# Kernel tuning notes

Hardware: AMD Instinct MI355X
Metric: run time of the kernel (lower is better)

The kernel has to match this reference:

```python
import jax, jax.numpy as jnp
import numpy as np

B, T, H, E, D, K = 4, 4096, 2048, 8, 1024, 2

def setup_inputs() -> dict:
    key = jax.random.key(0)
    ks = jax.random.split(key, 7)
    x  = jax.random.normal(ks[0], (B, T, H), dtype=jnp.float32)
    Wr = jax.random.normal(ks[1], (H, E), dtype=jnp.float32) * (1.0 / np.sqrt(H))
    br = jnp.zeros((E,), dtype=jnp.float32)
    We = jax.random.normal(ks[2], (E, H, D), dtype=jnp.float32) * (1.0 / np.sqrt(H))
    be = jnp.zeros((E, D), dtype=jnp.float32)
    Wc = jax.random.normal(ks[3], (D, H), dtype=jnp.float32) * (1.0 / np.sqrt(D))
    bc = jnp.zeros((H,), dtype=jnp.float32)
    return {"x": x, "Wr": Wr, "br": br, "We": We, "be": be, "Wc": Wc, "bc": bc}

def reference(x, Wr, br, We, be, Wc, bc):
    # Router: [B,T,H] @ [H,E] -> [B,T,E]
    router_logits = jnp.einsum('bth,he->bte', x, Wr) + br
    scores = jax.nn.softmax(router_logits, axis=-1)
    # top-k over experts (sorted descending, like torch.topk)
    topk_scores, topk_idx = jax.lax.top_k(scores, K)  # [B,T,K]
    # Dense all-expert linear: [B,T,E,D]
    expert_outs = jnp.einsum('bth,ehd->bted', x, We) + be
    # Gather the chosen experts per token: [B,T,K,D]
    gather_idx = jnp.broadcast_to(topk_idx[..., None], (B, T, K, D))
    chosen = jnp.take_along_axis(expert_outs, gather_idx, axis=2)
    # Weighted sum over top-k: [B,T,D]
    weighted = jnp.sum(chosen * topk_scores[..., None], axis=2)
    # Combine: [B,T,D] @ [D,H] -> [B,T,H]
    return jnp.einsum('btd,dh->bth', weighted, Wc) + bc
```

## Files before the change

### kernel.cpp

```cpp
#include <hip/hip_runtime.h>
#include <hip/hip_bf16.h>

typedef float f32x4 __attribute__((ext_vector_type(4)));
typedef short bf16x8 __attribute__((ext_vector_type(8)));

#define M_NT 16
#define M_OFF 17
#define M_TBL 32
#define MAX_TILES 264
#define NCHUNK 1024

__device__ __forceinline__ void gload16(const void* g, void* l) {
  __builtin_amdgcn_global_load_lds(
      (const __attribute__((address_space(1))) void*)g,
      (__attribute__((address_space(3))) void*)l, 16, 0, 0);
}

__device__ __forceinline__ float bf2f(unsigned short u) {
  union { unsigned int i; float f; } v; v.i = ((unsigned int)u) << 16; return v.f;
}
__device__ __forceinline__ unsigned short f2bf(float f) {
  __hip_bfloat16 h = __float2bfloat16(f);
  return __builtin_bit_cast(unsigned short, h);
}

__global__ void transpose_cvt(const float* __restrict__ src,
                              unsigned short* __restrict__ dst, int R, int C) {
  __shared__ float tile[32][33];
  int b = blockIdx.z;
  int c0 = blockIdx.x * 32, r0 = blockIdx.y * 32;
  src += (size_t)b * R * C;
  dst += (size_t)b * R * C;
  int tx = threadIdx.x, ty = threadIdx.y;
#pragma unroll
  for (int i = 0; i < 32; i += 8)
    tile[ty + i][tx] = src[(size_t)(r0 + ty + i) * C + c0 + tx];
  __syncthreads();
#pragma unroll
  for (int i = 0; i < 32; i += 8)
    dst[(size_t)(c0 + ty + i) * R + r0 + tx] = f2bf(tile[tx][ty + i]);
}

__global__ __launch_bounds__(256) void router_kernel(
    const float* __restrict__ x, const float* __restrict__ Wr,
    const float* __restrict__ br, unsigned short* __restrict__ xbf,
    float* __restrict__ scores, int* __restrict__ idx,
    int* __restrict__ blk_hist) {
  __shared__ int cnt[8];
  int tid = threadIdx.x, lane = tid & 63, w = tid >> 6;
  if (tid < 8) cnt[tid] = 0;
  __syncthreads();
  int t0 = blockIdx.x * 16 + w * 4;
  const float* xr = x + (size_t)t0 * 2048;
  unsigned short* xo = xbf + (size_t)t0 * 2048;
  float acc[4][8] = {};
#pragma unroll
  for (int j = 0; j < 8; ++j) {
    int h0 = j * 256 + lane * 4;
    float4 xv[4];
#pragma unroll
    for (int t = 0; t < 4; ++t) xv[t] = *(const float4*)(xr + (size_t)t * 2048 + h0);
#pragma unroll
    for (int t = 0; t < 4; ++t) {
      ushort4 p;
      p.x = f2bf(xv[t].x); p.y = f2bf(xv[t].y);
      p.z = f2bf(xv[t].z); p.w = f2bf(xv[t].w);
      *(ushort4*)(xo + (size_t)t * 2048 + h0) = p;
    }
    const float4* wp = (const float4*)(Wr + (size_t)h0 * 8);
#pragma unroll
    for (int c = 0; c < 4; ++c) {
      float4 w0 = wp[2 * c], w1 = wp[2 * c + 1];
      float xc0 = (c == 0) ? xv[0].x : (c == 1) ? xv[0].y : (c == 2) ? xv[0].z : xv[0].w;
      float xc1 = (c == 0) ? xv[1].x : (c == 1) ? xv[1].y : (c == 2) ? xv[1].z : xv[1].w;
      float xc2 = (c == 0) ? xv[2].x : (c == 1) ? xv[2].y : (c == 2) ? xv[2].z : xv[2].w;
      float xc3 = (c == 0) ? xv[3].x : (c == 1) ? xv[3].y : (c == 2) ? xv[3].z : xv[3].w;
      acc[0][0] += xc0 * w0.x; acc[0][1] += xc0 * w0.y; acc[0][2] += xc0 * w0.z; acc[0][3] += xc0 * w0.w;
      acc[0][4] += xc0 * w1.x; acc[0][5] += xc0 * w1.y; acc[0][6] += xc0 * w1.z; acc[0][7] += xc0 * w1.w;
      acc[1][0] += xc1 * w0.x; acc[1][1] += xc1 * w0.y; acc[1][2] += xc1 * w0.z; acc[1][3] += xc1 * w0.w;
      acc[1][4] += xc1 * w1.x; acc[1][5] += xc1 * w1.y; acc[1][6] += xc1 * w1.z; acc[1][7] += xc1 * w1.w;
      acc[2][0] += xc2 * w0.x; acc[2][1] += xc2 * w0.y; acc[2][2] += xc2 * w0.z; acc[2][3] += xc2 * w0.w;
      acc[2][4] += xc2 * w1.x; acc[2][5] += xc2 * w1.y; acc[2][6] += xc2 * w1.z; acc[2][7] += xc2 * w1.w;
      acc[3][0] += xc3 * w0.x; acc[3][1] += xc3 * w0.y; acc[3][2] += xc3 * w0.z; acc[3][3] += xc3 * w0.w;
      acc[3][4] += xc3 * w1.x; acc[3][5] += xc3 * w1.y; acc[3][6] += xc3 * w1.z; acc[3][7] += xc3 * w1.w;
    }
  }
#pragma unroll
  for (int t = 0; t < 4; ++t)
#pragma unroll
    for (int e = 0; e < 8; ++e)
#pragma unroll
      for (int off = 32; off > 0; off >>= 1)
        acc[t][e] += __shfl_xor(acc[t][e], off);
  if (lane < 4) {
    int t = t0 + lane;
    float l[8];
#pragma unroll
    for (int e = 0; e < 8; ++e) {
      float v = (lane == 0) ? acc[0][e] : (lane == 1) ? acc[1][e]
              : (lane == 2) ? acc[2][e] : acc[3][e];
      l[e] = v + br[e];
    }
    float mx = l[0];
#pragma unroll
    for (int e = 1; e < 8; ++e) mx = fmaxf(mx, l[e]);
    float se = 0.f;
#pragma unroll
    for (int e = 0; e < 8; ++e) se += __expf(l[e] - mx);
    float inv = 1.f / se;
    int e1 = 0; float b1 = l[0];
#pragma unroll
    for (int e = 1; e < 8; ++e) if (l[e] > b1) { b1 = l[e]; e1 = e; }
    int e2 = -1; float b2 = -1e30f;
#pragma unroll
    for (int e = 0; e < 8; ++e) if (e != e1 && l[e] > b2) { b2 = l[e]; e2 = e; }
    idx[2 * t] = e1; idx[2 * t + 1] = e2;
    scores[2 * t] = __expf(b1 - mx) * inv;
    scores[2 * t + 1] = __expf(b2 - mx) * inv;
    atomicAdd(&cnt[e1], 1);
    atomicAdd(&cnt[e2], 1);
  }
  __syncthreads();
  if (tid < 8) blk_hist[blockIdx.x * 8 + tid] = cnt[tid];
}

__global__ __launch_bounds__(512) void scan_kernel(
    const int* __restrict__ blk_hist, int* __restrict__ chunk_base,
    int* __restrict__ meta, int* __restrict__ rowlist) {
  __shared__ int stot[8], soff[8];
  int tid = threadIdx.x, lane = tid & 63, e = tid >> 6;
  int running = 0;
  for (int g = 0; g < NCHUNK / 64; ++g) {
    int c = g * 64 + lane;
    int v = blk_hist[c * 8 + e];
    int orig = v;
#pragma unroll
    for (int off = 1; off < 64; off <<= 1) {
      int n = __shfl_up(v, off);
      if (lane >= off) v += n;
    }
    chunk_base[c * 8 + e] = running + v - orig;
    running += __shfl(v, 63);
  }
  if (lane == 0) stot[e] = running;
  __syncthreads();
  if (tid == 0) {
    int off = 0, nt = 0;
    int4* tbl = (int4*)(meta + M_TBL);
    for (int ee = 0; ee < 8; ++ee) {
      int c = stot[ee];
      meta[M_OFF + ee] = off; soff[ee] = off;
      int tiles = (c + 127) >> 7;
      for (int t = 0; t < tiles; ++t)
        tbl[nt++] = make_int4(ee, off + t * 128, min(128, c - t * 128), 0);
      off += tiles << 7;
    }
    meta[M_NT] = nt;
  }
  __syncthreads();
  for (int ee = 0; ee < 8; ++ee) {
    int c = stot[ee], end = ((c + 127) >> 7) << 7;
    for (int i = c + tid; i < end; i += 512) rowlist[soff[ee] + i] = 0;
  }
}

__global__ void scatter_kernel(const int* __restrict__ idx,
                               const int* __restrict__ chunk_base,
                               const int* __restrict__ meta,
                               int* __restrict__ rowlist) {
  int c = blockIdx.x, lane = threadIdx.x;
  int entry = c * 32 + lane;
  int e = (lane < 32) ? idx[entry] : -1;
#pragma unroll
  for (int ee = 0; ee < 8; ++ee) {
    unsigned long long m = __ballot(e == ee);
    if (e == ee) {
      int rank = __popcll(m & ((1ull << lane) - 1));
      rowlist[meta[M_OFF + ee] + chunk_base[c * 8 + ee] + rank] = entry;
    }
  }
}

__global__ __launch_bounds__(256) void expert_gemm(
    const unsigned short* __restrict__ xbf,
    const unsigned short* __restrict__ WeT,
    const float* __restrict__ be,
    const float* __restrict__ scores,
    const int* __restrict__ rowlist,
    const int* __restrict__ meta,
    unsigned short* __restrict__ z) {
  __shared__ short lA[128 * 32];
  __shared__ short lB[128 * 32];
  __shared__ int lrows[128];
  if ((int)blockIdx.y >= meta[M_NT]) return;
  int4 tt = ((const int4*)(meta + M_TBL))[blockIdx.y];
  int e = tt.x, base = tt.y, valid = tt.z;
  int n0 = blockIdx.x * 128;
  int tid = threadIdx.x, lane = tid & 63, w = tid >> 6;
  if (tid < 128) lrows[tid] = rowlist[base + tid];
  __syncthreads();
  int ch0 = 2 * w, ch1 = ch0 + 1;
  int sub = lane >> 2, colb = (lane & 3) * 8;
  int ra0 = lrows[ch0 * 16 + sub] >> 1;
  int ra1 = lrows[ch1 * 16 + sub] >> 1;
  const unsigned short* sA0 = xbf + (size_t)ra0 * 2048 + colb;
  const unsigned short* sA1 = xbf + (size_t)ra1 * 2048 + colb;
  const unsigned short* Bb = WeT + (size_t)e * 1024 * 2048;
  const unsigned short* sB0 = Bb + (size_t)(n0 + ch0 * 16 + sub) * 2048 + colb;
  const unsigned short* sB1 = Bb + (size_t)(n0 + ch1 * 16 + sub) * 2048 + colb;
  f32x4 acc[4][4] = {};
  int wr = (w >> 1) * 64, wc = (w & 1) * 64;
  int fl = lane & 15, q = lane >> 4;
  for (int k0 = 0; k0 < 2048; k0 += 32) {
    __syncthreads();
    gload16(sA0, lA + ch0 * 512);
    gload16(sA1, lA + ch1 * 512);
    gload16(sB0, lB + ch0 * 512);
    gload16(sB1, lB + ch1 * 512);
    sA0 += 32; sA1 += 32; sB0 += 32; sB1 += 32;
    __syncthreads();
    bf16x8 a[4], b[4];
#pragma unroll
    for (int i = 0; i < 4; ++i) a[i] = *(const bf16x8*)(lA + (wr + i * 16 + fl) * 32 + q * 8);
#pragma unroll
    for (int i = 0; i < 4; ++i) b[i] = *(const bf16x8*)(lB + (wc + i * 16 + fl) * 32 + q * 8);
#pragma unroll
    for (int mi = 0; mi < 4; ++mi)
#pragma unroll
      for (int ni = 0; ni < 4; ++ni)
        acc[mi][ni] = __builtin_amdgcn_mfma_f32_16x16x32_bf16(a[mi], b[ni], acc[mi][ni], 0, 0, 0);
  }
  float bev[4];
#pragma unroll
  for (int ni = 0; ni < 4; ++ni) bev[ni] = be[e * 1024 + n0 + wc + ni * 16 + fl];
#pragma unroll
  for (int mi = 0; mi < 4; ++mi)
#pragma unroll
    for (int r = 0; r < 4; ++r) {
      int row = wr + mi * 16 + q * 4 + r;
      if (row < valid) {
        int entry = lrows[row];
        float s = scores[entry];
        unsigned short* zr = z + (size_t)entry * 1024 + n0 + wc;
#pragma unroll
        for (int ni = 0; ni < 4; ++ni)
          zr[ni * 16 + fl] = f2bf((acc[mi][ni][r] + bev[ni]) * s);
      }
    }
}

__global__ void wsum_kernel(const unsigned short* __restrict__ z,
                            unsigned short* __restrict__ y) {
  size_t i = ((size_t)blockIdx.x * 256 + threadIdx.x) * 8;
  size_t t = i >> 10, d = i & 1023;
  int4 za = *(const int4*)(z + (t * 2) * 1024 + d);
  int4 zb = *(const int4*)(z + (t * 2 + 1) * 1024 + d);
  int4 r;
  const unsigned short* pa = (const unsigned short*)&za;
  const unsigned short* pb = (const unsigned short*)&zb;
  unsigned short* pr = (unsigned short*)&r;
#pragma unroll
  for (int j = 0; j < 8; ++j) pr[j] = f2bf(bf2f(pa[j]) + bf2f(pb[j]));
  *(int4*)(y + i) = r;
}

__global__ __launch_bounds__(256) void combine_gemm(
    const unsigned short* __restrict__ y,
    const unsigned short* __restrict__ WcT,
    const float* __restrict__ bc,
    float* __restrict__ out) {
  __shared__ short lA[128 * 32];
  __shared__ short lB[128 * 32];
  int tid = threadIdx.x, lane = tid & 63, w = tid >> 6;
  int m0 = blockIdx.y * 128, n0 = blockIdx.x * 128;
  int ch0 = 2 * w, ch1 = ch0 + 1;
  int sub = lane >> 2, colb = (lane & 3) * 8;
  const unsigned short* sA0 = y + (size_t)(m0 + ch0 * 16 + sub) * 1024 + colb;
  const unsigned short* sA1 = y + (size_t)(m0 + ch1 * 16 + sub) * 1024 + colb;
  const unsigned short* sB0 = WcT + (size_t)(n0 + ch0 * 16 + sub) * 1024 + colb;
  const unsigned short* sB1 = WcT + (size_t)(n0 + ch1 * 16 + sub) * 1024 + colb;
  f32x4 acc[4][4] = {};
  int wr = (w >> 1) * 64, wc = (w & 1) * 64;
  int fl = lane & 15, q = lane >> 4;
  for (int k0 = 0; k0 < 1024; k0 += 32) {
    __syncthreads();
    gload16(sA0, lA + ch0 * 512);
    gload16(sA1, lA + ch1 * 512);
    gload16(sB0, lB + ch0 * 512);
    gload16(sB1, lB + ch1 * 512);
    sA0 += 32; sA1 += 32; sB0 += 32; sB1 += 32;
    __syncthreads();
    bf16x8 a[4], b[4];
#pragma unroll
    for (int i = 0; i < 4; ++i) a[i] = *(const bf16x8*)(lA + (wr + i * 16 + fl) * 32 + q * 8);
#pragma unroll
    for (int i = 0; i < 4; ++i) b[i] = *(const bf16x8*)(lB + (wc + i * 16 + fl) * 32 + q * 8);
#pragma unroll
    for (int mi = 0; mi < 4; ++mi)
#pragma unroll
      for (int ni = 0; ni < 4; ++ni)
        acc[mi][ni] = __builtin_amdgcn_mfma_f32_16x16x32_bf16(a[mi], b[ni], acc[mi][ni], 0, 0, 0);
  }
  float bcv[4];
#pragma unroll
  for (int ni = 0; ni < 4; ++ni) bcv[ni] = bc[n0 + wc + ni * 16 + fl];
#pragma unroll
  for (int mi = 0; mi < 4; ++mi)
#pragma unroll
    for (int r = 0; r < 4; ++r) {
      int row = m0 + wr + mi * 16 + q * 4 + r;
      float* orow = out + (size_t)row * 2048 + n0 + wc;
#pragma unroll
      for (int ni = 0; ni < 4; ++ni) orow[ni * 16 + fl] = acc[mi][ni][r] + bcv[ni];
    }
}

extern "C" void kernel_launch(void* const* d_in, const int* in_sizes, int n_in,
                              void* d_out, int out_size, void* d_ws, size_t ws_size,
                              hipStream_t stream) {
  const float* x  = (const float*)d_in[0];
  const float* Wr = (const float*)d_in[1];
  const float* br = (const float*)d_in[2];
  const float* We = (const float*)d_in[3];
  const float* be = (const float*)d_in[4];
  const float* Wc = (const float*)d_in[5];
  const float* bc = (const float*)d_in[6];
  float* out = (float*)d_out;

  char* ws = (char*)d_ws;
  size_t o = 0;
  auto alloc = [&](size_t b) {
    char* p = ws + o;
    o = (o + b + 255) & ~(size_t)255;
    return p;
  };
  unsigned short* xbf = (unsigned short*)alloc(16384UL * 2048 * 2);
  unsigned short* WeT = (unsigned short*)alloc(8UL * 1024 * 2048 * 2);
  unsigned short* WcT = (unsigned short*)alloc(2048UL * 1024 * 2);
  unsigned short* z   = (unsigned short*)alloc(32768UL * 1024 * 2);
  unsigned short* yw  = (unsigned short*)alloc(16384UL * 1024 * 2);
  float* scores = (float*)alloc(32768UL * 4);
  int* idx      = (int*)alloc(32768UL * 4);
  int* rowlist  = (int*)alloc(33792UL * 4);
  int* meta     = (int*)alloc(8192);
  int* blk_hist = (int*)alloc(NCHUNK * 8 * 4);
  int* chunk_base = (int*)alloc(NCHUNK * 8 * 4);
  (void)ws_size; (void)in_sizes; (void)n_in; (void)out_size;

  hipLaunchKernelGGL(transpose_cvt, dim3(32, 64, 8), dim3(32, 8), 0, stream, We, WeT, 2048, 1024);
  hipLaunchKernelGGL(transpose_cvt, dim3(64, 32, 1), dim3(32, 8), 0, stream, Wc, WcT, 1024, 2048);
  hipLaunchKernelGGL(router_kernel, dim3(NCHUNK), dim3(256), 0, stream, x, Wr, br, xbf, scores, idx, blk_hist);
  hipLaunchKernelGGL(scan_kernel, dim3(1), dim3(512), 0, stream, blk_hist, chunk_base, meta, rowlist);
  hipLaunchKernelGGL(scatter_kernel, dim3(NCHUNK), dim3(64), 0, stream, idx, chunk_base, meta, rowlist);
  hipLaunchKernelGGL(expert_gemm, dim3(8, MAX_TILES), dim3(256), 0, stream,
                     xbf, WeT, be, scores, rowlist, meta, z);
  hipLaunchKernelGGL(wsum_kernel, dim3(8192), dim3(256), 0, stream, z, yw);
  hipLaunchKernelGGL(combine_gemm, dim3(16, 128), dim3(256), 0, stream, yw, WcT, bc, out);
}
```

Measured before the change: 433.0 us.

## Rewrite MoE GEMMs with 256x128 tiles, double-buffered swizzled LDS, and grouped block ordering

Both the expert and combine GEMMs now use 512-thread blocks computing 256x128 tiles with a K-step of 64. Global-to-LDS loads are double-buffered and overlapped with MFMA work through explicit vmcnt waits and raw barriers, and the LDS layout is XOR-swizzled to avoid bank conflicts. Block indices are remapped so consecutive blocks share tiles for better L2 reuse, and the router table moves to 256-row tiles, which changes padding and the rowlist size. This is meant to cut the per-k-step sync overhead and the global latency stalls of the old single-buffer 128x128 loop, at the cost of more registers and padding waste on small expert groups.

```diff
diff --git a/kernel.cpp b/kernel.cpp
--- a/kernel.cpp
+++ b/kernel.cpp
@@ -7,7 +7,7 @@
 #define M_NT 16
 #define M_OFF 17
 #define M_TBL 32
-#define MAX_TILES 264
+#define MAX_TILES 136
 #define NCHUNK 1024
 
 __device__ __forceinline__ void gload16(const void* g, void* l) {
@@ -23,6 +23,10 @@
   __hip_bfloat16 h = __float2bfloat16(f);
   return __builtin_bit_cast(unsigned short, h);
 }
+
+#define CBAR() do { asm volatile("" ::: "memory"); __builtin_amdgcn_s_barrier(); asm volatile("" ::: "memory"); } while (0)
+#define VMC3() asm volatile("s_waitcnt vmcnt(3)" ::: "memory")
+#define VMC0() asm volatile("s_waitcnt vmcnt(0)" ::: "memory")
 
 __global__ void transpose_cvt(const float* __restrict__ src,
                               unsigned short* __restrict__ dst, int R, int C) {
@@ -150,16 +154,16 @@
     for (int ee = 0; ee < 8; ++ee) {
       int c = stot[ee];
       meta[M_OFF + ee] = off; soff[ee] = off;
-      int tiles = (c + 127) >> 7;
+      int tiles = (c + 255) >> 8;
       for (int t = 0; t < tiles; ++t)
-        tbl[nt++] = make_int4(ee, off + t * 128, min(128, c - t * 128), 0);
-      off += tiles << 7;
+        tbl[nt++] = make_int4(ee, off + t * 256, min(256, c - t * 256), 0);
+      off += tiles << 8;
     }
     meta[M_NT] = nt;
   }
   __syncthreads();
   for (int ee = 0; ee < 8; ++ee) {
-    int c = stot[ee], end = ((c + 127) >> 7) << 7;
+    int c = stot[ee], end = ((c + 255) >> 8) << 8;
     for (int i = c + tid; i < end; i += 512) rowlist[soff[ee] + i] = 0;
   }
 }
@@ -181,7 +185,29 @@
   }
 }
 
-__global__ __launch_bounds__(256) void expert_gemm(
+
+#define RD_FRAGS(AB, BB) do { \
+  _Pragma("unroll") for (int m_ = 0; m_ < 8; ++m_) \
+    av[m_] = *(const bf16x8*)(aP + (AB) + m_ * 1024); \
+  _Pragma("unroll") for (int n_ = 0; n_ < 2; ++n_) \
+    bv[n_] = *(const bf16x8*)(bP + (BB) + n_ * 1024); \
+} while (0)
+
+#define MFMA16() do { \
+  __builtin_amdgcn_s_setprio(1); \
+  _Pragma("unroll") for (int m_ = 0; m_ < 8; ++m_) \
+  _Pragma("unroll") for (int n_ = 0; n_ < 2; ++n_) \
+    acc[m_][n_] = __builtin_amdgcn_mfma_f32_16x16x32_bf16(av[m_], bv[n_], acc[m_][n_], 0, 0, 0); \
+  __builtin_amdgcn_s_setprio(0); \
+} while (0)
+
+#define STAGE(BUFB, KOFF) do { \
+  gload16(pA0 + (KOFF), dA + (BUFB)); \
+  gload16(pA1 + (KOFF), dA + (BUFB) + 8192); \
+  gload16(pB0 + (KOFF), dBs + (BUFB)); \
+} while (0)
+
+__global__ __launch_bounds__(512, 4) void expert_gemm(
     const unsigned short* __restrict__ xbf,
     const unsigned short* __restrict__ WeT,
     const float* __restrict__ be,
@@ -189,64 +215,127 @@
     const int* __restrict__ rowlist,
     const int* __restrict__ meta,
     unsigned short* __restrict__ z) {
-  __shared__ short lA[128 * 32];
-  __shared__ short lB[128 * 32];
-  __shared__ int lrows[128];
-  if ((int)blockIdx.y >= meta[M_NT]) return;
-  int4 tt = ((const int4*)(meta + M_TBL))[blockIdx.y];
+  __shared__ char smem[49152];
+  __shared__ int lrows[256];
+  int nt = meta[M_NT];
+  int flat = blockIdx.y * 8 + blockIdx.x;
+  int work = (flat & 7) * 136 + (flat >> 3);
+  int tileid = work >> 3, nb = work & 7;
+  if (tileid >= nt) return;
+  int4 tt = ((const int4*)(meta + M_TBL))[tileid];
   int e = tt.x, base = tt.y, valid = tt.z;
-  int n0 = blockIdx.x * 128;
+  int n0 = nb * 128;
   int tid = threadIdx.x, lane = tid & 63, w = tid >> 6;
-  if (tid < 128) lrows[tid] = rowlist[base + tid];
-  __syncthreads();
-  int ch0 = 2 * w, ch1 = ch0 + 1;
-  int sub = lane >> 2, colb = (lane & 3) * 8;
-  int ra0 = lrows[ch0 * 16 + sub] >> 1;
-  int ra1 = lrows[ch1 * 16 + sub] >> 1;
-  const unsigned short* sA0 = xbf + (size_t)ra0 * 2048 + colb;
-  const unsigned short* sA1 = xbf + (size_t)ra1 * 2048 + colb;
-  const unsigned short* Bb = WeT + (size_t)e * 1024 * 2048;
-  const unsigned short* sB0 = Bb + (size_t)(n0 + ch0 * 16 + sub) * 2048 + colb;
-  const unsigned short* sB1 = Bb + (size_t)(n0 + ch1 * 16 + sub) * 2048 + colb;
-  f32x4 acc[4][4] = {};
-  int wr = (w >> 1) * 64, wc = (w & 1) * 64;
+  if (tid < 256) lrows[tid] = rowlist[base + tid];
+  __syncthreads();
+  int wm = w >> 2, wn = w & 3;
   int fl = lane & 15, q = lane >> 4;
-  for (int k0 = 0; k0 < 2048; k0 += 32) {
-    __syncthreads();
-    gload16(sA0, lA + ch0 * 512);
-    gload16(sA1, lA + ch1 * 512);
-    gload16(sB0, lB + ch0 * 512);
-    gload16(sB1, lB + ch1 * 512);
-    sA0 += 32; sA1 += 32; sB0 += 32; sB1 += 32;
-    __syncthreads();
-    bf16x8 a[4], b[4];
-#pragma unroll
-    for (int i = 0; i < 4; ++i) a[i] = *(const bf16x8*)(lA + (wr + i * 16 + fl) * 32 + q * 8);
-#pragma unroll
-    for (int i = 0; i < 4; ++i) b[i] = *(const bf16x8*)(lB + (wc + i * 16 + fl) * 32 + q * 8);
-#pragma unroll
-    for (int mi = 0; mi < 4; ++mi)
-#pragma unroll
-      for (int ni = 0; ni < 4; ++ni)
-        acc[mi][ni] = __builtin_amdgcn_mfma_f32_16x16x32_bf16(a[mi], b[ni], acc[mi][ni], 0, 0, 0);
-  }
-  float bev[4];
-#pragma unroll
-  for (int ni = 0; ni < 4; ++ni) bev[ni] = be[e * 1024 + n0 + wc + ni * 16 + fl];
-#pragma unroll
-  for (int mi = 0; mi < 4; ++mi)
+  int rA = tid >> 2;
+  int sl = ((tid & 3) ^ (rA & 3)) * 16;
+  const char* pA0 = (const char*)xbf + (size_t)(lrows[rA] >> 1) * 4096 + sl;
+  const char* pA1 = (const char*)xbf + (size_t)(lrows[rA + 128] >> 1) * 4096 + sl;
+  const char* pB0 = (const char*)WeT + ((size_t)e * 1024 + n0 + rA) * 4096 + sl;
+  char* dA  = smem + tid * 16;
+  char* dBs = smem + 16384 + tid * 16;
+  int swz = (fl & 3) << 4;
+  const char* aP = smem + (wm * 128 + fl) * 64 + ((q * 16) ^ swz);
+  const char* bP = smem + 16384 + (wn * 32 + fl) * 64 + ((q * 16) ^ swz);
+  STAGE(0, 0); STAGE(24576, 64);
+  VMC3(); CBAR();
+  f32x4 acc[8][2] = {};
+  bf16x8 av[8], bv[2];
+  const int NT = 64;
+  for (int t2 = 0; t2 < NT; t2 += 2) {
+    int koff = t2 * 64;
+    RD_FRAGS(0, 0);
+    MFMA16();
+    CBAR();
+    if (t2 + 2 < NT) { STAGE(0, koff + 128); VMC3(); } else { VMC0(); }
+    CBAR();
+    RD_FRAGS(24576, 24576);
+    MFMA16();
+    CBAR();
+    if (t2 + 3 < NT) { STAGE(24576, koff + 192); VMC3(); } else { VMC0(); }
+    CBAR();
+  }
+  float bev[2];
+#pragma unroll
+  for (int nc = 0; nc < 2; ++nc)
+    bev[nc] = be[e * 1024 + n0 + wn * 32 + nc * 16 + fl];
+#pragma unroll
+  for (int mi = 0; mi < 8; ++mi) {
+    int rowbase = wm * 128 + mi * 16 + q * 4;
 #pragma unroll
     for (int r = 0; r < 4; ++r) {
-      int row = wr + mi * 16 + q * 4 + r;
+      int row = rowbase + r;
       if (row < valid) {
         int entry = lrows[row];
         float s = scores[entry];
-        unsigned short* zr = z + (size_t)entry * 1024 + n0 + wc;
-#pragma unroll
-        for (int ni = 0; ni < 4; ++ni)
-          zr[ni * 16 + fl] = f2bf((acc[mi][ni][r] + bev[ni]) * s);
+        unsigned short* zr = z + (size_t)entry * 1024 + n0 + wn * 32 + fl;
+#pragma unroll
+        for (int nc = 0; nc < 2; ++nc)
+          zr[nc * 16] = f2bf((acc[mi][nc][r] + bev[nc]) * s);
       }
     }
+  }
+}
+
+__global__ __launch_bounds__(512, 4) void combine_gemm(
+    const unsigned short* __restrict__ y,
+    const unsigned short* __restrict__ WcT,
+    const float* __restrict__ bc,
+    float* __restrict__ out) {
+  __shared__ char smem[49152];
+  int flat = blockIdx.y * 8 + blockIdx.x;
+  int work = (flat & 7) * 128 + (flat >> 3);
+  int mtile = work >> 4, nb = work & 15;
+  int m0 = mtile * 256, n0 = nb * 128;
+  int tid = threadIdx.x, lane = tid & 63, w = tid >> 6;
+  int wm = w >> 2, wn = w & 3;
+  int fl = lane & 15, q = lane >> 4;
+  int rA = tid >> 2;
+  int sl = ((tid & 3) ^ (rA & 3)) * 16;
+  const char* pA0 = (const char*)y + (size_t)(m0 + rA) * 2048 + sl;
+  const char* pA1 = (const char*)y + (size_t)(m0 + rA + 128) * 2048 + sl;
+  const char* pB0 = (const char*)WcT + (size_t)(n0 + rA) * 2048 + sl;
+  char* dA  = smem + tid * 16;
+  char* dBs = smem + 16384 + tid * 16;
+  int swz = (fl & 3) << 4;
+  const char* aP = smem + (wm * 128 + fl) * 64 + ((q * 16) ^ swz);
+  const char* bP = smem + 16384 + (wn * 32 + fl) * 64 + ((q * 16) ^ swz);
+  STAGE(0, 0); STAGE(24576, 64);
+  VMC3(); CBAR();
+  f32x4 acc[8][2] = {};
+  bf16x8 av[8], bv[2];
+  const int NT = 32;
+  for (int t2 = 0; t2 < NT; t2 += 2) {
+    int koff = t2 * 64;
+    RD_FRAGS(0, 0);
+    MFMA16();
+    CBAR();
+    if (t2 + 2 < NT) { STAGE(0, koff + 128); VMC3(); } else { VMC0(); }
+    CBAR();
+    RD_FRAGS(24576, 24576);
+    MFMA16();
+    CBAR();
+    if (t2 + 3 < NT) { STAGE(24576, koff + 192); VMC3(); } else { VMC0(); }
+    CBAR();
+  }
+  float bcv[2];
+#pragma unroll
+  for (int nc = 0; nc < 2; ++nc)
+    bcv[nc] = bc[n0 + wn * 32 + nc * 16 + fl];
+#pragma unroll
+  for (int mi = 0; mi < 8; ++mi) {
+    int rowbase = m0 + wm * 128 + mi * 16 + q * 4;
+#pragma unroll
+    for (int r = 0; r < 4; ++r) {
+      float* orow = out + (size_t)(rowbase + r) * 2048 + n0 + wn * 32 + fl;
+#pragma unroll
+      for (int nc = 0; nc < 2; ++nc)
+        orow[nc * 16] = acc[mi][nc][r] + bcv[nc];
+    }
+  }
 }
 
 __global__ void wsum_kernel(const unsigned short* __restrict__ z,
@@ -262,57 +351,6 @@
 #pragma unroll
   for (int j = 0; j < 8; ++j) pr[j] = f2bf(bf2f(pa[j]) + bf2f(pb[j]));
   *(int4*)(y + i) = r;
-}
-
-__global__ __launch_bounds__(256) void combine_gemm(
-    const unsigned short* __restrict__ y,
-    const unsigned short* __restrict__ WcT,
-    const float* __restrict__ bc,
-    float* __restrict__ out) {
-  __shared__ short lA[128 * 32];
-  __shared__ short lB[128 * 32];
-  int tid = threadIdx.x, lane = tid & 63, w = tid >> 6;
-  int m0 = blockIdx.y * 128, n0 = blockIdx.x * 128;
-  int ch0 = 2 * w, ch1 = ch0 + 1;
-  int sub = lane >> 2, colb = (lane & 3) * 8;
-  const unsigned short* sA0 = y + (size_t)(m0 + ch0 * 16 + sub) * 1024 + colb;
-  const unsigned short* sA1 = y + (size_t)(m0 + ch1 * 16 + sub) * 1024 + colb;
-  const unsigned short* sB0 = WcT + (size_t)(n0 + ch0 * 16 + sub) * 1024 + colb;
-  const unsigned short* sB1 = WcT + (size_t)(n0 + ch1 * 16 + sub) * 1024 + colb;
-  f32x4 acc[4][4] = {};
-  int wr = (w >> 1) * 64, wc = (w & 1) * 64;
-  int fl = lane & 15, q = lane >> 4;
-  for (int k0 = 0; k0 < 1024; k0 += 32) {
-    __syncthreads();
-    gload16(sA0, lA + ch0 * 512);
-    gload16(sA1, lA + ch1 * 512);
-    gload16(sB0, lB + ch0 * 512);
-    gload16(sB1, lB + ch1 * 512);
-    sA0 += 32; sA1 += 32; sB0 += 32; sB1 += 32;
-    __syncthreads();
-    bf16x8 a[4], b[4];
-#pragma unroll
-    for (int i = 0; i < 4; ++i) a[i] = *(const bf16x8*)(lA + (wr + i * 16 + fl) * 32 + q * 8);
-#pragma unroll
-    for (int i = 0; i < 4; ++i) b[i] = *(const bf16x8*)(lB + (wc + i * 16 + fl) * 32 + q * 8);
-#pragma unroll
-    for (int mi = 0; mi < 4; ++mi)
-#pragma unroll
-      for (int ni = 0; ni < 4; ++ni)
-        acc[mi][ni] = __builtin_amdgcn_mfma_f32_16x16x32_bf16(a[mi], b[ni], acc[mi][ni], 0, 0, 0);
-  }
-  float bcv[4];
-#pragma unroll
-  for (int ni = 0; ni < 4; ++ni) bcv[ni] = bc[n0 + wc + ni * 16 + fl];
-#pragma unroll
-  for (int mi = 0; mi < 4; ++mi)
-#pragma unroll
-    for (int r = 0; r < 4; ++r) {
-      int row = m0 + wr + mi * 16 + q * 4 + r;
-      float* orow = out + (size_t)row * 2048 + n0 + wc;
-#pragma unroll
-      for (int ni = 0; ni < 4; ++ni) orow[ni * 16 + fl] = acc[mi][ni][r] + bcv[ni];
-    }
 }
 
 extern "C" void kernel_launch(void* const* d_in, const int* in_sizes, int n_in,
@@ -341,7 +379,7 @@
   unsigned short* yw  = (unsigned short*)alloc(16384UL * 1024 * 2);
   float* scores = (float*)alloc(32768UL * 4);
   int* idx      = (int*)alloc(32768UL * 4);
-  int* rowlist  = (int*)alloc(33792UL * 4);
+  int* rowlist  = (int*)alloc(36864UL * 4);
   int* meta     = (int*)alloc(8192);
   int* blk_hist = (int*)alloc(NCHUNK * 8 * 4);
   int* chunk_base = (int*)alloc(NCHUNK * 8 * 4);
@@ -352,8 +390,8 @@
   hipLaunchKernelGGL(router_kernel, dim3(NCHUNK), dim3(256), 0, stream, x, Wr, br, xbf, scores, idx, blk_hist);
   hipLaunchKernelGGL(scan_kernel, dim3(1), dim3(512), 0, stream, blk_hist, chunk_base, meta, rowlist);
   hipLaunchKernelGGL(scatter_kernel, dim3(NCHUNK), dim3(64), 0, stream, idx, chunk_base, meta, rowlist);
-  hipLaunchKernelGGL(expert_gemm, dim3(8, MAX_TILES), dim3(256), 0, stream,
+  hipLaunchKernelGGL(expert_gemm, dim3(8, MAX_TILES), dim3(512), 0, stream,
                      xbf, WeT, be, scores, rowlist, meta, z);
   hipLaunchKernelGGL(wsum_kernel, dim3(8192), dim3(256), 0, stream, z, yw);
-  hipLaunchKernelGGL(combine_gemm, dim3(16, 128), dim3(256), 0, stream, yw, WcT, bc, out);
-}
+  hipLaunchKernelGGL(combine_gemm, dim3(8, 128), dim3(512), 0, stream, yw, WcT, bc, out);
+}
```

Measured after the change: 395.1 us. 8.8% less time.

## Replace LDS-staged GEMMs with single-wave direct-register double-buffered MFMA kernels

Applied to the files above, without the earlier changes.

Both expert and combine GEMMs drop LDS staging and block-wide barriers. Each 64-thread wave now loads its own 128x64 operand fragments straight from global memory into registers, double-buffers them, and raises wave priority around the MFMA bursts. Expert tiles grow to 256 rows, and the flat grid is remapped so work spreads across XCDs. This removes synchronisation and LDS traffic, but gives up operand sharing between waves, so global/L2 load traffic and register pressure rise.

```diff
diff --git a/kernel.cpp b/kernel.cpp
--- a/kernel.cpp
+++ b/kernel.cpp
@@ -7,14 +7,8 @@
 #define M_NT 16
 #define M_OFF 17
 #define M_TBL 32
-#define MAX_TILES 264
+#define MAX_TILES 136
 #define NCHUNK 1024
-
-__device__ __forceinline__ void gload16(const void* g, void* l) {
-  __builtin_amdgcn_global_load_lds(
-      (const __attribute__((address_space(1))) void*)g,
-      (__attribute__((address_space(3))) void*)l, 16, 0, 0);
-}
 
 __device__ __forceinline__ float bf2f(unsigned short u) {
   union { unsigned int i; float f; } v; v.i = ((unsigned int)u) << 16; return v.f;
@@ -150,16 +144,16 @@
     for (int ee = 0; ee < 8; ++ee) {
       int c = stot[ee];
       meta[M_OFF + ee] = off; soff[ee] = off;
-      int tiles = (c + 127) >> 7;
+      int tiles = (c + 255) >> 8;
       for (int t = 0; t < tiles; ++t)
-        tbl[nt++] = make_int4(ee, off + t * 128, min(128, c - t * 128), 0);
-      off += tiles << 7;
+        tbl[nt++] = make_int4(ee, off + t * 256, min(256, c - t * 256), 0);
+      off += tiles << 8;
     }
     meta[M_NT] = nt;
   }
   __syncthreads();
   for (int ee = 0; ee < 8; ++ee) {
-    int c = stot[ee], end = ((c + 127) >> 7) << 7;
+    int c = stot[ee], end = ((c + 255) >> 8) << 8;
     for (int i = c + tid; i < end; i += 512) rowlist[soff[ee] + i] = 0;
   }
 }
@@ -181,7 +175,25 @@
   }
 }
 
-__global__ __launch_bounds__(256) void expert_gemm(
+
+#define RLOAD(AV, BV) do { \
+  _Pragma("unroll") for (int m_ = 0; m_ < 8; ++m_) \
+    AV[m_] = *(const bf16x8*)(aBase + ao[m_]); \
+  _Pragma("unroll") for (int n_ = 0; n_ < 4; ++n_) \
+    BV[n_] = *(const bf16x8*)(bBase + bo[n_]); \
+  _Pragma("unroll") for (int m_ = 0; m_ < 8; ++m_) ao[m_] += 64u; \
+  _Pragma("unroll") for (int n_ = 0; n_ < 4; ++n_) bo[n_] += 64u; \
+} while (0)
+
+#define RMFMA(AV, BV) do { \
+  __builtin_amdgcn_s_setprio(1); \
+  _Pragma("unroll") for (int m_ = 0; m_ < 8; ++m_) \
+  _Pragma("unroll") for (int n_ = 0; n_ < 4; ++n_) \
+    acc[m_][n_] = __builtin_amdgcn_mfma_f32_16x16x32_bf16(AV[m_], BV[n_], acc[m_][n_], 0, 0, 0); \
+  __builtin_amdgcn_s_setprio(0); \
+} while (0)
+
+__global__ __launch_bounds__(64, 2) void expert_gemm(
     const unsigned short* __restrict__ xbf,
     const unsigned short* __restrict__ WeT,
     const float* __restrict__ be,
@@ -189,64 +201,108 @@
     const int* __restrict__ rowlist,
     const int* __restrict__ meta,
     unsigned short* __restrict__ z) {
-  __shared__ short lA[128 * 32];
-  __shared__ short lB[128 * 32];
-  __shared__ int lrows[128];
-  if ((int)blockIdx.y >= meta[M_NT]) return;
-  int4 tt = ((const int4*)(meta + M_TBL))[blockIdx.y];
+  int nt = meta[M_NT];
+  int flat = blockIdx.x;
+  int work = (flat & 7) * 544 + (flat >> 3);
+  int tileid = work >> 5;
+  if (tileid >= nt) return;
+  int sub = work & 31, wm = sub >> 4, nb = sub & 15;
+  int4 tt = ((const int4*)(meta + M_TBL))[tileid];
   int e = tt.x, base = tt.y, valid = tt.z;
-  int n0 = blockIdx.x * 128;
-  int tid = threadIdx.x, lane = tid & 63, w = tid >> 6;
-  if (tid < 128) lrows[tid] = rowlist[base + tid];
-  __syncthreads();
-  int ch0 = 2 * w, ch1 = ch0 + 1;
-  int sub = lane >> 2, colb = (lane & 3) * 8;
-  int ra0 = lrows[ch0 * 16 + sub] >> 1;
-  int ra1 = lrows[ch1 * 16 + sub] >> 1;
-  const unsigned short* sA0 = xbf + (size_t)ra0 * 2048 + colb;
-  const unsigned short* sA1 = xbf + (size_t)ra1 * 2048 + colb;
-  const unsigned short* Bb = WeT + (size_t)e * 1024 * 2048;
-  const unsigned short* sB0 = Bb + (size_t)(n0 + ch0 * 16 + sub) * 2048 + colb;
-  const unsigned short* sB1 = Bb + (size_t)(n0 + ch1 * 16 + sub) * 2048 + colb;
-  f32x4 acc[4][4] = {};
-  int wr = (w >> 1) * 64, wc = (w & 1) * 64;
-  int fl = lane & 15, q = lane >> 4;
-  for (int k0 = 0; k0 < 2048; k0 += 32) {
-    __syncthreads();
-    gload16(sA0, lA + ch0 * 512);
-    gload16(sA1, lA + ch1 * 512);
-    gload16(sB0, lB + ch0 * 512);
-    gload16(sB1, lB + ch1 * 512);
-    sA0 += 32; sA1 += 32; sB0 += 32; sB1 += 32;
-    __syncthreads();
-    bf16x8 a[4], b[4];
-#pragma unroll
-    for (int i = 0; i < 4; ++i) a[i] = *(const bf16x8*)(lA + (wr + i * 16 + fl) * 32 + q * 8);
-#pragma unroll
-    for (int i = 0; i < 4; ++i) b[i] = *(const bf16x8*)(lB + (wc + i * 16 + fl) * 32 + q * 8);
-#pragma unroll
-    for (int mi = 0; mi < 4; ++mi)
-#pragma unroll
-      for (int ni = 0; ni < 4; ++ni)
-        acc[mi][ni] = __builtin_amdgcn_mfma_f32_16x16x32_bf16(a[mi], b[ni], acc[mi][ni], 0, 0, 0);
-  }
+  int n0 = nb * 64;
+  int lane = threadIdx.x, fl = lane & 15, q = lane >> 4;
+  const int* rl = rowlist + base + wm * 128;
+  const char* aBase = (const char*)xbf;
+  const char* bBase = (const char*)WeT;
+  unsigned ao[8], bo[4];
+#pragma unroll
+  for (int m = 0; m < 8; ++m)
+    ao[m] = (unsigned)(rl[m * 16 + fl] >> 1) * 4096u + q * 16u;
+#pragma unroll
+  for (int n = 0; n < 4; ++n)
+    bo[n] = (unsigned)(e * 1024 + n0 + n * 16 + fl) * 4096u + q * 16u;
+  f32x4 acc[8][4] = {};
+  bf16x8 a0[8], b0[4], a1[8], b1[4];
+  RLOAD(a0, b0);
+  RLOAD(a1, b1);
+  const int NT = 64;
+  for (int t = 0; t < NT - 2; t += 2) {
+    RMFMA(a0, b0);
+    RLOAD(a0, b0);
+    RMFMA(a1, b1);
+    RLOAD(a1, b1);
+  }
+  RMFMA(a0, b0);
+  RMFMA(a1, b1);
   float bev[4];
 #pragma unroll
-  for (int ni = 0; ni < 4; ++ni) bev[ni] = be[e * 1024 + n0 + wc + ni * 16 + fl];
-#pragma unroll
-  for (int mi = 0; mi < 4; ++mi)
+  for (int n = 0; n < 4; ++n)
+    bev[n] = be[e * 1024 + n0 + n * 16 + fl];
+#pragma unroll
+  for (int m = 0; m < 8; ++m) {
+    int rowbase = wm * 128 + m * 16 + q * 4;
 #pragma unroll
     for (int r = 0; r < 4; ++r) {
-      int row = wr + mi * 16 + q * 4 + r;
+      int row = rowbase + r;
       if (row < valid) {
-        int entry = lrows[row];
+        int entry = rowlist[base + row];
         float s = scores[entry];
-        unsigned short* zr = z + (size_t)entry * 1024 + n0 + wc;
-#pragma unroll
-        for (int ni = 0; ni < 4; ++ni)
-          zr[ni * 16 + fl] = f2bf((acc[mi][ni][r] + bev[ni]) * s);
+        unsigned short* zr = z + (size_t)entry * 1024 + n0 + fl;
+#pragma unroll
+        for (int n = 0; n < 4; ++n)
+          zr[n * 16] = f2bf((acc[m][n][r] + bev[n]) * s);
       }
     }
+  }
+}
+
+__global__ __launch_bounds__(64, 2) void combine_gemm(
+    const unsigned short* __restrict__ y,
+    const unsigned short* __restrict__ WcT,
+    const float* __restrict__ bc,
+    float* __restrict__ out) {
+  int flat = blockIdx.x;
+  int work = (flat & 7) * 512 + (flat >> 3);
+  int mt = work >> 5, nb = work & 31;
+  int m0 = mt * 128, n0 = nb * 64;
+  int lane = threadIdx.x, fl = lane & 15, q = lane >> 4;
+  const char* aBase = (const char*)y;
+  const char* bBase = (const char*)WcT;
+  unsigned ao[8], bo[4];
+#pragma unroll
+  for (int m = 0; m < 8; ++m)
+    ao[m] = (unsigned)(m0 + m * 16 + fl) * 2048u + q * 16u;
+#pragma unroll
+  for (int n = 0; n < 4; ++n)
+    bo[n] = (unsigned)(n0 + n * 16 + fl) * 2048u + q * 16u;
+  f32x4 acc[8][4] = {};
+  bf16x8 a0[8], b0[4], a1[8], b1[4];
+  RLOAD(a0, b0);
+  RLOAD(a1, b1);
+  const int NT = 32;
+  for (int t = 0; t < NT - 2; t += 2) {
+    RMFMA(a0, b0);
+    RLOAD(a0, b0);
+    RMFMA(a1, b1);
+    RLOAD(a1, b1);
+  }
+  RMFMA(a0, b0);
+  RMFMA(a1, b1);
+  float bcv[4];
+#pragma unroll
+  for (int n = 0; n < 4; ++n)
+    bcv[n] = bc[n0 + n * 16 + fl];
+#pragma unroll
+  for (int m = 0; m < 8; ++m) {
+    int rowbase = m0 + m * 16 + q * 4;
+#pragma unroll
+    for (int r = 0; r < 4; ++r) {
+      float* orow = out + (size_t)(rowbase + r) * 2048 + n0 + fl;
+#pragma unroll
+      for (int n = 0; n < 4; ++n)
+        orow[n * 16] = acc[m][n][r] + bcv[n];
+    }
+  }
 }
 
 __global__ void wsum_kernel(const unsigned short* __restrict__ z,
@@ -262,57 +318,6 @@
 #pragma unroll
   for (int j = 0; j < 8; ++j) pr[j] = f2bf(bf2f(pa[j]) + bf2f(pb[j]));
   *(int4*)(y + i) = r;
-}
-
-__global__ __launch_bounds__(256) void combine_gemm(
-    const unsigned short* __restrict__ y,
-    const unsigned short* __restrict__ WcT,
-    const float* __restrict__ bc,
-    float* __restrict__ out) {
-  __shared__ short lA[128 * 32];
-  __shared__ short lB[128 * 32];
-  int tid = threadIdx.x, lane = tid & 63, w = tid >> 6;
-  int m0 = blockIdx.y * 128, n0 = blockIdx.x * 128;
-  int ch0 = 2 * w, ch1 = ch0 + 1;
-  int sub = lane >> 2, colb = (lane & 3) * 8;
-  const unsigned short* sA0 = y + (size_t)(m0 + ch0 * 16 + sub) * 1024 + colb;
-  const unsigned short* sA1 = y + (size_t)(m0 + ch1 * 16 + sub) * 1024 + colb;
-  const unsigned short* sB0 = WcT + (size_t)(n0 + ch0 * 16 + sub) * 1024 + colb;
-  const unsigned short* sB1 = WcT + (size_t)(n0 + ch1 * 16 + sub) * 1024 + colb;
-  f32x4 acc[4][4] = {};
-  int wr = (w >> 1) * 64, wc = (w & 1) * 64;
-  int fl = lane & 15, q = lane >> 4;
-  for (int k0 = 0; k0 < 1024; k0 += 32) {
-    __syncthreads();
-    gload16(sA0, lA + ch0 * 512);
-    gload16(sA1, lA + ch1 * 512);
-    gload16(sB0, lB + ch0 * 512);
-    gload16(sB1, lB + ch1 * 512);
-    sA0 += 32; sA1 += 32; sB0 += 32; sB1 += 32;
-    __syncthreads();
-    bf16x8 a[4], b[4];
-#pragma unroll
-    for (int i = 0; i < 4; ++i) a[i] = *(const bf16x8*)(lA + (wr + i * 16 + fl) * 32 + q * 8);
-#pragma unroll
-    for (int i = 0; i < 4; ++i) b[i] = *(const bf16x8*)(lB + (wc + i * 16 + fl) * 32 + q * 8);
-#pragma unroll
-    for (int mi = 0; mi < 4; ++mi)
-#pragma unroll
-      for (int ni = 0; ni < 4; ++ni)
-        acc[mi][ni] = __builtin_amdgcn_mfma_f32_16x16x32_bf16(a[mi], b[ni], acc[mi][ni], 0, 0, 0);
-  }
-  float bcv[4];
-#pragma unroll
-  for (int ni = 0; ni < 4; ++ni) bcv[ni] = bc[n0 + wc + ni * 16 + fl];
-#pragma unroll
-  for (int mi = 0; mi < 4; ++mi)
-#pragma unroll
-    for (int r = 0; r < 4; ++r) {
-      int row = m0 + wr + mi * 16 + q * 4 + r;
-      float* orow = out + (size_t)row * 2048 + n0 + wc;
-#pragma unroll
-      for (int ni = 0; ni < 4; ++ni) orow[ni * 16 + fl] = acc[mi][ni][r] + bcv[ni];
-    }
 }
 
 extern "C" void kernel_launch(void* const* d_in, const int* in_sizes, int n_in,
@@ -341,7 +346,7 @@
   unsigned short* yw  = (unsigned short*)alloc(16384UL * 1024 * 2);
   float* scores = (float*)alloc(32768UL * 4);
   int* idx      = (int*)alloc(32768UL * 4);
-  int* rowlist  = (int*)alloc(33792UL * 4);
+  int* rowlist  = (int*)alloc(36864UL * 4);
   int* meta     = (int*)alloc(8192);
   int* blk_hist = (int*)alloc(NCHUNK * 8 * 4);
   int* chunk_base = (int*)alloc(NCHUNK * 8 * 4);
@@ -352,8 +357,8 @@
   hipLaunchKernelGGL(router_kernel, dim3(NCHUNK), dim3(256), 0, stream, x, Wr, br, xbf, scores, idx, blk_hist);
   hipLaunchKernelGGL(scan_kernel, dim3(1), dim3(512), 0, stream, blk_hist, chunk_base, meta, rowlist);
   hipLaunchKernelGGL(scatter_kernel, dim3(NCHUNK), dim3(64), 0, stream, idx, chunk_base, meta, rowlist);
-  hipLaunchKernelGGL(expert_gemm, dim3(8, MAX_TILES), dim3(256), 0, stream,
+  hipLaunchKernelGGL(expert_gemm, dim3(MAX_TILES * 32), dim3(64), 0, stream,
                      xbf, WeT, be, scores, rowlist, meta, z);
   hipLaunchKernelGGL(wsum_kernel, dim3(8192), dim3(256), 0, stream, z, yw);
-  hipLaunchKernelGGL(combine_gemm, dim3(16, 128), dim3(256), 0, stream, yw, WcT, bc, out);
-}
+  hipLaunchKernelGGL(combine_gemm, dim3(4096), dim3(64), 0, stream, yw, WcT, bc, out);
+}
```

After: 765.0 us. 76.7% more time.
